# Kernel tuning notes

Measured on AMD Instinct MI355X. Metric: run time of the kernel, lower is better.

## Reference

```python
import jax, jax.numpy as jnp
import numpy as np
from jax import lax

D_MODEL, D_INNER, D_STATE, DT_RANK, KG, DCONV = 96, 96, 64, 6, 4, 3
BATCH, SEQ = 4, 16384


def setup_inputs() -> dict:
    ks = jax.random.split(jax.random.key(0), 8)
    x = jax.random.normal(ks[0], (BATCH, SEQ, D_MODEL), jnp.float32)
    in_proj_w = jax.random.normal(ks[1], (2 * D_INNER, D_MODEL), jnp.float32) * (D_MODEL ** -0.5)
    conv_w = jax.random.normal(ks[2], (D_INNER, 1, DCONV), jnp.float32) * (DCONV ** -0.5)
    x_proj_w = jax.random.normal(ks[3], (KG, DT_RANK + 2 * D_STATE, D_INNER), jnp.float32) * (D_INNER ** -0.5)
    dt_projs_w = 0.1 * jax.random.uniform(ks[4], (KG, D_INNER, DT_RANK), jnp.float32)
    out_proj_w = jax.random.normal(ks[5], (D_MODEL, D_INNER), jnp.float32) * (D_INNER ** -0.5)
    A_logs = 0.1 * jax.random.uniform(ks[6], (KG * D_INNER, D_STATE), jnp.float32)
    Ds = jnp.ones((KG * D_INNER,), jnp.float32)
    return dict(x=x, in_proj_w=in_proj_w, conv_w=conv_w, x_proj_w=x_proj_w,
                dt_projs_w=dt_projs_w, out_proj_w=out_proj_w, A_logs=A_logs, Ds=Ds)


def _forward_core(x, x_proj_w, dt_projs_w, A_logs, Ds):
    # x: (B, L, Din). 4-direction stack: [fwd, rev, fwd, rev] as in torch code.
    B, L, Din = x.shape
    x_rev = jnp.flip(x, axis=1)
    xs = jnp.stack([x, x_rev, x, x_rev], axis=1)                      # (B, K, L, Din)
    x_dbl = jnp.einsum('bkld,kcd->bklc', xs, x_proj_w)                # (B, K, L, R+2N)
    dts, Bs, Cs = jnp.split(x_dbl, [DT_RANK, DT_RANK + D_STATE], axis=-1)
    dts = jnp.einsum('bklr,kdr->bkld', dts, dt_projs_w)               # (B, K, L, Din)
    delta = jax.nn.softplus(dts)                                      # delta_bias is zeros in source
    A = -jnp.exp(A_logs).reshape(KG, D_INNER, D_STATE)                # (K, Din, N)
    D = Ds.reshape(KG, D_INNER)

    def step(h, inp):
        d, u, b, c = inp                                              # d,u:(B,K,Din)  b,c:(B,K,N)
        dA = jnp.exp(d[..., None] * A)                                # (B,K,Din,N)
        h = dA * h + (d * u)[..., None] * b[:, :, None, :]
        y = jnp.einsum('bkdn,bkn->bkd', h, c)
        return h, y

    seq = (jnp.moveaxis(delta, 2, 0), jnp.moveaxis(xs, 2, 0),
           jnp.moveaxis(Bs, 2, 0), jnp.moveaxis(Cs, 2, 0))
    h0 = jnp.zeros((B, KG, D_INNER, D_STATE), x.dtype)
    _, ys = lax.scan(step, h0, seq)                                   # (L, B, K, Din)
    ys = jnp.moveaxis(ys, 0, 2) + D[None, :, None, :] * xs            # (B, K, L, Din)
    # cross-merge: un-flip the reversed directions and sum all 4
    y = ys[:, 0] + jnp.flip(ys[:, 1], axis=1) + ys[:, 2] + jnp.flip(ys[:, 3], axis=1)
    return y                                                          # (B, L, Din)


def reference(x, in_proj_w, conv_w, x_proj_w, dt_projs_w, out_proj_w, A_logs, Ds):
    xz = x @ in_proj_w.T                                              # (B, L, 2*Din)
    xx, z = jnp.split(xz, 2, axis=-1)
    z = jax.nn.gelu(z, approximate=False)
    # depthwise conv1d over the sequence dim, 'same' padding
    pad = (DCONV - 1) // 2
    xc = lax.conv_general_dilated(xx.transpose(0, 2, 1), conv_w, (1,), [(pad, pad)],
                                  dimension_numbers=('NCH', 'OIH', 'NCH'),
                                  feature_group_count=D_INNER)        # (B, Din, L)
    xx = jax.nn.gelu(xc.transpose(0, 2, 1), approximate=False)        # (B, L, Din)
    y = _forward_core(xx, x_proj_w, dt_projs_w, A_logs, Ds)
    y = y * z
    return y @ out_proj_w.T                                           # (B, L, d_model)
```

## Files before the change

kernel.cpp:

```cpp
#include <hip/hip_runtime.h>
#include <hip/hip_bf16.h>
#include <math.h>

#define B_    4
#define L_    16384
#define DM    96
#define DI    96
#define NS    64
#define RK    6
#define KG_   4
#define CDIM  134

#define CL    512
#define NC    32
#define NWARM 64
#define STG   32

typedef float f32x2 __attribute__((ext_vector_type(2)));
typedef float f32x4 __attribute__((ext_vector_type(4)));
typedef short bf16x8 __attribute__((ext_vector_type(8)));

#if defined(__has_builtin)
# if __has_builtin(__builtin_amdgcn_exp2f)
#  define EXP2F(x) __builtin_amdgcn_exp2f(x)
# else
#  define EXP2F(x) exp2f(x)
# endif
#else
# define EXP2F(x) exp2f(x)
#endif

__device__ __forceinline__ float gelu_f(float v) {
  return 0.5f * v * (1.0f + erff(v * 0.70710678118654752f));
}

__device__ __forceinline__ unsigned short f2bf(float v) {
  __hip_bfloat16 h = __float2bfloat16(v);
  return *reinterpret_cast<unsigned short*>(&h);
}

__global__ __launch_bounds__(256) void k_front(
    const float* __restrict__ x, const float* __restrict__ w,
    const float* __restrict__ cw,
    float* __restrict__ xxc, float* __restrict__ zg)
{
  __shared__ __align__(16) char smem[80 * 104 * 2 + 96 * 104 * 2];
  unsigned short* sxb = reinterpret_cast<unsigned short*>(smem);
  unsigned short* swb = reinterpret_cast<unsigned short*>(smem + 80 * 104 * 2);
  const int tid = threadIdx.x;
  const int lt = blockIdx.x, cs = blockIdx.y, b = blockIdx.z;
  const int l0 = lt * 64;
  const int lbase = l0 - 1;

  for (int i = tid; i < 80 * 24; i += 256) {
    const int r = i / 24, q = i % 24;
    int l = lbase + r; l = l < 0 ? 0 : (l >= L_ ? L_ - 1 : l);
    const float4 v = reinterpret_cast<const float4*>(x + ((size_t)b * L_ + l) * DM)[q];
    ushort4 u;
    u.x = f2bf(v.x); u.y = f2bf(v.y); u.z = f2bf(v.z); u.w = f2bf(v.w);
    *reinterpret_cast<ushort4*>(&sxb[r * 104 + q * 4]) = u;
  }
  const float* wp = w + (size_t)cs * 96 * DM;
  for (int i = tid; i < 96 * 24; i += 256) {
    const int r = i / 24, q = i % 24;
    const float4 v = reinterpret_cast<const float4*>(wp + (size_t)r * DM)[q];
    ushort4 u;
    u.x = f2bf(v.x); u.y = f2bf(v.y); u.z = f2bf(v.z); u.w = f2bf(v.w);
    *reinterpret_cast<ushort4*>(&swb[r * 104 + q * 4]) = u;
  }
  __syncthreads();

  const int wv = tid >> 6, lane = tid & 63;
  const int lrow = lane & 15, lkg = lane >> 4;
  f32x4 acc[8];
#pragma unroll
  for (int i = 0; i < 8; ++i) {
    acc[i] = (f32x4){0.f, 0.f, 0.f, 0.f};
    const int tile = wv + 4 * i;
    if (tile < 30) {
      const int mt = tile / 6, nt = tile - mt * 6;
#pragma unroll
      for (int kk = 0; kk < 3; ++kk) {
        const int kbase = kk * 32 + lkg * 8;
        const bf16x8 af = *reinterpret_cast<const bf16x8*>(&sxb[(mt * 16 + lrow) * 104 + kbase]);
        const bf16x8 bfm = *reinterpret_cast<const bf16x8*>(&swb[(nt * 16 + lrow) * 104 + kbase]);
        acc[i] = __builtin_amdgcn_mfma_f32_16x16x32_bf16(af, bfm, acc[i], 0, 0, 0);
      }
    }
  }
  __syncthreads();

  float* sprod = reinterpret_cast<float*>(smem);
#pragma unroll
  for (int i = 0; i < 8; ++i) {
    const int tile = wv + 4 * i;
    if (tile < 30) {
      const int mt = tile / 6, nt = tile - mt * 6;
      const int row = mt * 16 + lkg * 4;
      const int col = nt * 16 + lrow;
#pragma unroll
      for (int reg = 0; reg < 4; ++reg)
        sprod[(row + reg) * 100 + col] = acc[i][reg];
    }
  }
  __syncthreads();

  if (cs == 0) {
    float* op = xxc + ((size_t)b * L_ + l0) * DI;
    for (int i = tid; i < 64 * 24; i += 256) {
      const int ro = i / 24, q = i % 24;
      const int lo = l0 + ro;
      const float4 xm4 = *reinterpret_cast<const float4*>(&sprod[ro * 100 + q * 4]);
      const float4 x04 = *reinterpret_cast<const float4*>(&sprod[(ro + 1) * 100 + q * 4]);
      const float4 xq4 = *reinterpret_cast<const float4*>(&sprod[(ro + 2) * 100 + q * 4]);
      const float mzero = (lo > 0) ? 1.f : 0.f;
      const float qzero = (lo < L_ - 1) ? 1.f : 0.f;
      float4 o;
      {
        const int d0 = q * 4;
        const float* c = cw + d0 * 3;
        o.x = gelu_f(c[0] * xm4.x * mzero + c[1]  * x04.x + c[2]  * xq4.x * qzero);
        o.y = gelu_f(c[3] * xm4.y * mzero + c[4]  * x04.y + c[5]  * xq4.y * qzero);
        o.z = gelu_f(c[6] * xm4.z * mzero + c[7]  * x04.z + c[8]  * xq4.z * qzero);
        o.w = gelu_f(c[9] * xm4.w * mzero + c[10] * x04.w + c[11] * xq4.w * qzero);
      }
      reinterpret_cast<float4*>(op + (size_t)ro * DI)[q] = o;
    }
  } else {
    float* op = zg + ((size_t)b * L_ + l0) * DI;
    for (int i = tid; i < 64 * 24; i += 256) {
      const int ro = i / 24, q = i % 24;
      const float4 v = *reinterpret_cast<const float4*>(&sprod[(ro + 1) * 100 + q * 4]);
      float4 o;
      o.x = gelu_f(v.x); o.y = gelu_f(v.y); o.z = gelu_f(v.z); o.w = gelu_f(v.w);
      reinterpret_cast<float4*>(op + (size_t)ro * DI)[q] = o;
    }
  }
}

__global__ __launch_bounds__(256) void k_xproj(
    const float* __restrict__ xxc, const float* __restrict__ xpw,
    const float* __restrict__ dtw,
    __hip_bfloat16* __restrict__ delta, __hip_bfloat16* __restrict__ Bs,
    __hip_bfloat16* __restrict__ Cs)
{
  __shared__ __align__(16) unsigned short sxb[64][104];
  __shared__ __align__(16) unsigned short swb[144 * 104];
  __shared__ __align__(16) float sdtw[576];
  const int tid = threadIdx.x;
  const int lt = blockIdx.x, kdir = blockIdx.y, b = blockIdx.z;
  const int l0 = lt * 64;
  const bool rev = (kdir & 1) != 0;

  for (int i = tid; i < 576; i += 256) sdtw[i] = dtw[(size_t)kdir * 576 + i];

  for (int i = tid; i < 64 * 24; i += 256) {
    const int r = i / 24, q = i % 24;
    const int l = l0 + r;
    const int p = rev ? (L_ - 1 - l) : l;
    const float4 v = reinterpret_cast<const float4*>(xxc + ((size_t)b * L_ + p) * DI)[q];
    ushort4 u;
    u.x = f2bf(v.x); u.y = f2bf(v.y); u.z = f2bf(v.z); u.w = f2bf(v.w);
    *reinterpret_cast<ushort4*>(&sxb[r][q * 4]) = u;
  }
  const float* wp = xpw + (size_t)kdir * CDIM * DI;
  for (int i = tid; i < 144 * 24; i += 256) {
    const int r = i / 24, q = i % 24;
    float4 v = make_float4(0.f, 0.f, 0.f, 0.f);
    if (r < CDIM) v = reinterpret_cast<const float4*>(wp + (size_t)r * DI)[q];
    ushort4 u;
    u.x = f2bf(v.x); u.y = f2bf(v.y); u.z = f2bf(v.z); u.w = f2bf(v.w);
    *reinterpret_cast<ushort4*>(&swb[r * 104 + q * 4]) = u;
  }
  __syncthreads();

  const int wv = tid >> 6, lane = tid & 63;
  const int m0 = wv * 16;
  const int lrow = lane & 15, lkg = lane >> 4;
  f32x4 acc[9];
#pragma unroll
  for (int n = 0; n < 9; ++n) acc[n] = (f32x4){0.f, 0.f, 0.f, 0.f};

#pragma unroll
  for (int kk = 0; kk < 3; ++kk) {
    const int kbase = kk * 32 + lkg * 8;
    const bf16x8 af = *reinterpret_cast<const bf16x8*>(&sxb[m0 + lrow][kbase]);
#pragma unroll
    for (int n = 0; n < 9; ++n) {
      const bf16x8 bfm = *reinterpret_cast<const bf16x8*>(&swb[(n * 16 + lrow) * 104 + kbase]);
      acc[n] = __builtin_amdgcn_mfma_f32_16x16x32_bf16(af, bfm, acc[n], 0, 0, 0);
    }
  }
  __syncthreads();

  unsigned short* soB = swb;
  unsigned short* soC = swb + 64 * 68;
  float* sdts = reinterpret_cast<float*>(swb + 2 * 64 * 68);

  {
    const int row = m0 + lkg * 4;
#pragma unroll
    for (int n = 0; n < 9; ++n) {
      const int c = n * 16 + lrow;
#pragma unroll
      for (int reg = 0; reg < 4; ++reg) {
        const float v = acc[n][reg];
        const int rr = row + reg;
        if (c < RK)            sdts[rr * 8 + c] = v;
        else if (c < RK + NS)  soB[rr * 68 + (c - RK)] = f2bf(v);
        else if (c < CDIM)     soC[rr * 68 + (c - RK - NS)] = f2bf(v);
      }
    }
  }
  __syncthreads();

  const size_t bk = (size_t)(b * KG_ + kdir);
  {
    unsigned short* bsg = reinterpret_cast<unsigned short*>(Bs);
    unsigned short* csg = reinterpret_cast<unsigned short*>(Cs);
    const size_t nbase = (bk * L_ + l0) * NS;
    for (int i = tid; i < 64 * 16; i += 256) {
      const int r = i >> 4, q = i & 15;
      const ushort4 vb = *reinterpret_cast<const ushort4*>(&soB[r * 68 + q * 4]);
      const ushort4 vc = *reinterpret_cast<const ushort4*>(&soC[r * 68 + q * 4]);
      *reinterpret_cast<ushort4*>(bsg + nbase + (size_t)r * NS + q * 4) = vb;
      *reinterpret_cast<ushort4*>(csg + nbase + (size_t)r * NS + q * 4) = vc;
    }
  }
  {
    unsigned short* dg = reinterpret_cast<unsigned short*>(delta);
    const size_t dbase = (bk * L_ + l0) * DI;
    for (int i = tid; i < 64 * 24; i += 256) {
      const int r = i / 24, q = i - r * 24;
      const int dc0 = q * 4;
      ushort4 u;
      float o[4];
#pragma unroll
      for (int e = 0; e < 4; ++e) {
        const int dc = dc0 + e;
        float s = 0.f;
#pragma unroll
        for (int rr6 = 0; rr6 < RK; ++rr6)
          s += sdts[r * 8 + rr6] * sdtw[dc * RK + rr6];
        o[e] = (s > 20.f) ? s : log1pf(__expf(s));
      }
      u.x = f2bf(o[0]); u.y = f2bf(o[1]); u.z = f2bf(o[2]); u.w = f2bf(o[3]);
      *reinterpret_cast<ushort4*>(dg + dbase + (size_t)r * DI + dc0) = u;
    }
  }
}

__global__ __launch_bounds__(768) void k_scan(
    const float* __restrict__ xxc,
    const __hip_bfloat16* __restrict__ delta,
    const __hip_bfloat16* __restrict__ Bs,
    const __hip_bfloat16* __restrict__ Cs,
    const float* __restrict__ A_logs, const float* __restrict__ Ds,
    float* __restrict__ ysum)
{
  __shared__ __align__(16) float s_du[STG][192];
  __shared__ __align__(16) float s_u[STG][96];
  __shared__ __align__(16) float s_B[STG][64];
  __shared__ __align__(16) float s_C[STG][64];
  __shared__ __align__(16) float s_y[STG][96];
  const int tid = threadIdx.x;
  const int ci = blockIdx.x, k = blockIdx.y, b = blockIdx.z;
  const int d = tid >> 3, j = tid & 7;
  const int jn = j * 8;
  const bool rev = (k & 1) != 0;
  const float LOG2E = 1.4426950408889634f;

  const int r96 = tid / 96;
  const int c96 = tid - r96 * 96;
  const int r64 = tid >> 6;
  const int c64 = tid & 63;

  f32x2 a2[4], h[4];
#pragma unroll
  for (int p = 0; p < 4; ++p) {
    const int n = jn + 2 * p;
    a2[p].x = -__expf(A_logs[((size_t)(k * DI + d)) * NS + n])     * LOG2E;
    a2[p].y = -__expf(A_logs[((size_t)(k * DI + d)) * NS + n + 1]) * LOG2E;
    h[p].x = 0.f; h[p].y = 0.f;
  }
  const float Dc = Ds[k * DI + c96];

  const int emit0 = ci * CL;
  const int lstart = (emit0 - NWARM > 0) ? (emit0 - NWARM) : 0;
  const int lend = emit0 + CL;
  const size_t bk = (size_t)(b * KG_ + k);

  for (int s = lstart; s < lend; s += STG) {
    __syncthreads();
    {
      const size_t dbase = (bk * L_ + s) * DI;
      const int pbase = rev ? (L_ - 1 - s) : s;
      const int psgn  = rev ? -1 : 1;
      const float* ubase = xxc + ((size_t)b * L_ + pbase) * DI + c96;
#pragma unroll
      for (int it = 0; it < 4; ++it) {
        const int t = r96 + 8 * it;
        const float dl = __bfloat162float(delta[dbase + (size_t)t * DI + c96]);
        const float uu = ubase[(ptrdiff_t)psgn * t * DI];
        f32x2 v; v.x = dl; v.y = dl * uu;
        *(f32x2*)&s_du[t][2 * c96] = v;
        s_u[t][c96] = uu;
      }
      const size_t nbase = (bk * L_ + s) * NS;
#pragma unroll
      for (int it = 0; it < 3; ++it) {
        const int t = r64 + 12 * it;
        if (t < STG) {
          s_B[t][c64] = __bfloat162float(Bs[nbase + (size_t)t * NS + c64]);
          s_C[t][c64] = __bfloat162float(Cs[nbase + (size_t)t * NS + c64]);
        }
      }
    }
    __syncthreads();
    const bool emit = (s >= emit0);
#pragma unroll 8
    for (int t = 0; t < STG; ++t) {
      const f32x2 du = *(const f32x2*)&s_du[t][2 * d];
      const float dlt = du.x, bu = du.y;
      const f32x2 dlt2 = {dlt, dlt};
      const f32x2 bu2 = {bu, bu};
      const f32x4 Bv0 = *(const f32x4*)&s_B[t][jn];
      const f32x4 Bv1 = *(const f32x4*)&s_B[t][jn + 4];
      const f32x4 Cv0 = *(const f32x4*)&s_C[t][jn];
      const f32x4 Cv1 = *(const f32x4*)&s_C[t][jn + 4];
      const f32x2 bp[4] = {{Bv0.x, Bv0.y}, {Bv0.z, Bv0.w},
                           {Bv1.x, Bv1.y}, {Bv1.z, Bv1.w}};
      const f32x2 cp[4] = {{Cv0.x, Cv0.y}, {Cv0.z, Cv0.w},
                           {Cv1.x, Cv1.y}, {Cv1.z, Cv1.w}};
      f32x2 y2 = {0.f, 0.f};
#pragma unroll
      for (int p = 0; p < 4; ++p) {
        const f32x2 arg = dlt2 * a2[p];
        f32x2 e;
        e.x = EXP2F(arg.x);
        e.y = EXP2F(arg.y);
        h[p] = e * h[p] + bu2 * bp[p];
        y2 += h[p] * cp[p];
      }
      float y = y2.x + y2.y;
      y += __shfl_xor(y, 1);
      y += __shfl_xor(y, 2);
      y += __shfl_xor(y, 4);
      if (emit && j == 0) s_y[t][d] = y;
    }
    if (emit) {
      __syncthreads();
      const int pbase = rev ? (L_ - 1 - s) : s;
      const int psgn  = rev ? -1 : 1;
      float* ybase = ysum + ((size_t)b * L_ + pbase) * DI + c96;
#pragma unroll
      for (int it = 0; it < 4; ++it) {
        const int t = r96 + 8 * it;
        atomicAdd(ybase + (ptrdiff_t)psgn * t * DI,
                  fmaf(Dc, s_u[t][c96], s_y[t][c96]));
      }
    }
  }
}

__global__ __launch_bounds__(256) void k_out(
    const float* __restrict__ ysum, const float* __restrict__ zg,
    const float* __restrict__ wout, float* __restrict__ out)
{
  __shared__ __align__(16) char smem[64 * 104 * 2 + 96 * 104 * 2];
  unsigned short* sab = reinterpret_cast<unsigned short*>(smem);
  unsigned short* swb = reinterpret_cast<unsigned short*>(smem + 64*104*2);
  const int tid = threadIdx.x;
  const int lt = blockIdx.x, b = blockIdx.y;
  const int l0 = lt * 64;
  const size_t rbase = ((size_t)b * L_ + l0) * DI;

  for (int i = tid; i < 64 * 24; i += 256) {
    const int r = i / 24, q = i % 24;
    float4 av = reinterpret_cast<const float4*>(ysum + rbase + (size_t)r * DI)[q];
    const float4 zv = reinterpret_cast<const float4*>(zg + rbase + (size_t)r * DI)[q];
    ushort4 u;
    u.x = f2bf(av.x * zv.x); u.y = f2bf(av.y * zv.y);
    u.z = f2bf(av.z * zv.z); u.w = f2bf(av.w * zv.w);
    *reinterpret_cast<ushort4*>(&sab[r * 104 + q * 4]) = u;
  }
  for (int i = tid; i < 96 * 24; i += 256) {
    const int r = i / 24, q = i % 24;
    const float4 v = reinterpret_cast<const float4*>(wout + (size_t)r * DM)[q];
    ushort4 u;
    u.x = f2bf(v.x); u.y = f2bf(v.y); u.z = f2bf(v.z); u.w = f2bf(v.w);
    *reinterpret_cast<ushort4*>(&swb[r * 104 + q * 4]) = u;
  }
  __syncthreads();

  const int wv = tid >> 6, lane = tid & 63;
  const int m0 = wv * 16;
  const int lrow = lane & 15, lkg = lane >> 4;
  f32x4 acc[6];
#pragma unroll
  for (int n = 0; n < 6; ++n) acc[n] = (f32x4){0.f, 0.f, 0.f, 0.f};

#pragma unroll
  for (int kk = 0; kk < 3; ++kk) {
    const int kbase = kk * 32 + lkg * 8;
    const bf16x8 af = *reinterpret_cast<const bf16x8*>(&sab[(m0 + lrow) * 104 + kbase]);
#pragma unroll
    for (int n = 0; n < 6; ++n) {
      const bf16x8 bfm = *reinterpret_cast<const bf16x8*>(&swb[(n * 16 + lrow) * 104 + kbase]);
      acc[n] = __builtin_amdgcn_mfma_f32_16x16x32_bf16(af, bfm, acc[n], 0, 0, 0);
    }
  }
  __syncthreads();

  float* sout = reinterpret_cast<float*>(smem);
  {
    const int row = m0 + lkg * 4;
#pragma unroll
    for (int n = 0; n < 6; ++n) {
      const int c = n * 16 + lrow;
#pragma unroll
      for (int reg = 0; reg < 4; ++reg)
        sout[(row + reg) * 100 + c] = acc[n][reg];
    }
  }
  __syncthreads();

  float* op = out + ((size_t)b * L_ + l0) * DM;
  for (int i = tid; i < 64 * 24; i += 256) {
    const int r = i / 24, q = i % 24;
    const float4 v = *reinterpret_cast<const float4*>(&sout[r * 100 + q * 4]);
    reinterpret_cast<float4*>(op + (size_t)r * DM)[q] = v;
  }
}

extern "C" void kernel_launch(void* const* d_in, const int* in_sizes, int n_in,
                              void* d_out, int out_size, void* d_ws, size_t ws_size,
                              hipStream_t stream)
{
  const float* x    = (const float*)d_in[0];
  const float* ipw  = (const float*)d_in[1];
  const float* cw   = (const float*)d_in[2];
  const float* xpw  = (const float*)d_in[3];
  const float* dtw  = (const float*)d_in[4];
  const float* opw  = (const float*)d_in[5];
  const float* alog = (const float*)d_in[6];
  const float* dsv  = (const float*)d_in[7];
  float* out = (float*)d_out;
  char* ws = (char*)d_ws;

  const size_t SZ_XZ  = (size_t)B_ * L_ * 192 * 4;
  const size_t SZ_F   = (size_t)B_ * L_ * DI * 4;
  const size_t SZ_NBF = (size_t)B_ * KG_ * L_ * NS * 2;

  __hip_bfloat16* dlt  = (__hip_bfloat16*)ws;
  float* xxc           = (float*)(ws + SZ_XZ);
  float* zgp           = (float*)(ws + SZ_XZ + SZ_F);
  __hip_bfloat16* Bsp  = (__hip_bfloat16*)(ws + SZ_XZ + 2 * SZ_F);
  __hip_bfloat16* Csp  = (__hip_bfloat16*)(ws + SZ_XZ + 2 * SZ_F + SZ_NBF);
  float* ysum          = (float*)(ws + SZ_XZ + 2 * SZ_F + 2 * SZ_NBF);

  hipMemsetAsync(ysum, 0, SZ_F, stream);
  k_front  <<<dim3(L_ / 64, 2, B_),   256, 0, stream>>>(x, ipw, cw, xxc, zgp);
  k_xproj  <<<dim3(L_ / 64, KG_, B_), 256, 0, stream>>>(xxc, xpw, dtw, dlt, Bsp, Csp);
  k_scan   <<<dim3(NC, KG_, B_),      768, 0, stream>>>(xxc, dlt, Bsp, Csp, alog, dsv, ysum);
  k_out    <<<dim3(L_ / 64, B_),      256, 0, stream>>>(ysum, zgp, opw, out);
}
```

Measured before the change: 480.0 us.

## Fuse in-projection, conv and x-projection into a single front kernel

Merges k_front and k_xproj into one kernel. Each block now computes both the x and z halves of the in-projection, then the conv+GELU, and keeps the conv output in LDS as bf16. It then loops over the four scan directions, handling reversed directions by remapping rows instead of re-reading flipped xxc from global memory. This removes a kernel launch, the global re-read of xxc (four times), and the duplicate x-tile loading across the two channel halves. In exchange the grid shrinks to a quarter, LDS use per block rises to about 57 KB, and the direction loop serialises the x_proj weight loads with extra barriers, which lowers occupancy and parallelism.

```diff
diff --git a/kernel.cpp b/kernel.cpp
--- a/kernel.cpp
+++ b/kernel.cpp
@@ -39,18 +39,24 @@
   return *reinterpret_cast<unsigned short*>(&h);
 }
 
-__global__ __launch_bounds__(256) void k_front(
+__global__ __launch_bounds__(256) void k_fx(
     const float* __restrict__ x, const float* __restrict__ w,
-    const float* __restrict__ cw,
-    float* __restrict__ xxc, float* __restrict__ zg)
+    const float* __restrict__ cw, const float* __restrict__ xpw,
+    const float* __restrict__ dtw,
+    float* __restrict__ xxc, float* __restrict__ zg,
+    __hip_bfloat16* __restrict__ delta, __hip_bfloat16* __restrict__ Bs,
+    __hip_bfloat16* __restrict__ Cs)
 {
-  __shared__ __align__(16) char smem[80 * 104 * 2 + 96 * 104 * 2];
-  unsigned short* sxb = reinterpret_cast<unsigned short*>(smem);
-  unsigned short* swb = reinterpret_cast<unsigned short*>(smem + 80 * 104 * 2);
+  __shared__ __align__(16) char smem[57600];
+  unsigned short* sxb  = reinterpret_cast<unsigned short*>(smem);
+  unsigned short* swbX = reinterpret_cast<unsigned short*>(smem + 16640);
+  unsigned short* swbZ = reinterpret_cast<unsigned short*>(smem + 36608);
   const int tid = threadIdx.x;
-  const int lt = blockIdx.x, cs = blockIdx.y, b = blockIdx.z;
+  const int lt = blockIdx.x, b = blockIdx.y;
   const int l0 = lt * 64;
   const int lbase = l0 - 1;
+  const int wv = tid >> 6, lane = tid & 63;
+  const int lrow = lane & 15, lkg = lane >> 4;
 
   for (int i = tid; i < 80 * 24; i += 256) {
     const int r = i / 24, q = i % 24;
@@ -60,22 +66,23 @@
     u.x = f2bf(v.x); u.y = f2bf(v.y); u.z = f2bf(v.z); u.w = f2bf(v.w);
     *reinterpret_cast<ushort4*>(&sxb[r * 104 + q * 4]) = u;
   }
-  const float* wp = w + (size_t)cs * 96 * DM;
   for (int i = tid; i < 96 * 24; i += 256) {
     const int r = i / 24, q = i % 24;
-    const float4 v = reinterpret_cast<const float4*>(wp + (size_t)r * DM)[q];
-    ushort4 u;
-    u.x = f2bf(v.x); u.y = f2bf(v.y); u.z = f2bf(v.z); u.w = f2bf(v.w);
-    *reinterpret_cast<ushort4*>(&swb[r * 104 + q * 4]) = u;
-  }
-  __syncthreads();
-
-  const int wv = tid >> 6, lane = tid & 63;
-  const int lrow = lane & 15, lkg = lane >> 4;
-  f32x4 acc[8];
+    const float4 vx = reinterpret_cast<const float4*>(w + (size_t)r * DM)[q];
+    const float4 vz = reinterpret_cast<const float4*>(w + (size_t)(96 + r) * DM)[q];
+    ushort4 ux, uz;
+    ux.x = f2bf(vx.x); ux.y = f2bf(vx.y); ux.z = f2bf(vx.z); ux.w = f2bf(vx.w);
+    uz.x = f2bf(vz.x); uz.y = f2bf(vz.y); uz.z = f2bf(vz.z); uz.w = f2bf(vz.w);
+    *reinterpret_cast<ushort4*>(&swbX[r * 104 + q * 4]) = ux;
+    *reinterpret_cast<ushort4*>(&swbZ[r * 104 + q * 4]) = uz;
+  }
+  __syncthreads();
+
+  f32x4 accX[8], accZ[8];
 #pragma unroll
   for (int i = 0; i < 8; ++i) {
-    acc[i] = (f32x4){0.f, 0.f, 0.f, 0.f};
+    accX[i] = (f32x4){0.f, 0.f, 0.f, 0.f};
+    accZ[i] = (f32x4){0.f, 0.f, 0.f, 0.f};
     const int tile = wv + 4 * i;
     if (tile < 30) {
       const int mt = tile / 6, nt = tile - mt * 6;
@@ -83,14 +90,17 @@
       for (int kk = 0; kk < 3; ++kk) {
         const int kbase = kk * 32 + lkg * 8;
         const bf16x8 af = *reinterpret_cast<const bf16x8*>(&sxb[(mt * 16 + lrow) * 104 + kbase]);
-        const bf16x8 bfm = *reinterpret_cast<const bf16x8*>(&swb[(nt * 16 + lrow) * 104 + kbase]);
-        acc[i] = __builtin_amdgcn_mfma_f32_16x16x32_bf16(af, bfm, acc[i], 0, 0, 0);
-      }
-    }
-  }
-  __syncthreads();
-
-  float* sprod = reinterpret_cast<float*>(smem);
+        const bf16x8 bx = *reinterpret_cast<const bf16x8*>(&swbX[(nt * 16 + lrow) * 104 + kbase]);
+        const bf16x8 bz = *reinterpret_cast<const bf16x8*>(&swbZ[(nt * 16 + lrow) * 104 + kbase]);
+        accX[i] = __builtin_amdgcn_mfma_f32_16x16x32_bf16(af, bx, accX[i], 0, 0, 0);
+        accZ[i] = __builtin_amdgcn_mfma_f32_16x16x32_bf16(af, bz, accZ[i], 0, 0, 0);
+      }
+    }
+  }
+  __syncthreads();
+
+  float* prodX = reinterpret_cast<float*>(smem);
+  float* prodZ = reinterpret_cast<float*>(smem + 32000);
 #pragma unroll
   for (int i = 0; i < 8; ++i) {
     const int tile = wv + 4 * i;
@@ -99,20 +109,36 @@
       const int row = mt * 16 + lkg * 4;
       const int col = nt * 16 + lrow;
 #pragma unroll
-      for (int reg = 0; reg < 4; ++reg)
-        sprod[(row + reg) * 100 + col] = acc[i][reg];
-    }
-  }
-  __syncthreads();
-
-  if (cs == 0) {
+      for (int reg = 0; reg < 4; ++reg) {
+        prodX[(row + reg) * 100 + col] = accX[i][reg];
+        const int zr = row + reg - 1;
+        if (zr >= 0 && zr < 64) prodZ[zr * 100 + col] = accZ[i][reg];
+      }
+    }
+  }
+  __syncthreads();
+
+  {
+    float* op = zg + ((size_t)b * L_ + l0) * DI;
+    for (int i = tid; i < 64 * 24; i += 256) {
+      const int ro = i / 24, q = i % 24;
+      const float4 v = *reinterpret_cast<const float4*>(&prodZ[ro * 100 + q * 4]);
+      float4 o;
+      o.x = gelu_f(v.x); o.y = gelu_f(v.y); o.z = gelu_f(v.z); o.w = gelu_f(v.w);
+      reinterpret_cast<float4*>(op + (size_t)ro * DI)[q] = o;
+    }
+  }
+  __syncthreads();
+
+  unsigned short* sxc = reinterpret_cast<unsigned short*>(smem + 32000);
+  {
     float* op = xxc + ((size_t)b * L_ + l0) * DI;
     for (int i = tid; i < 64 * 24; i += 256) {
       const int ro = i / 24, q = i % 24;
       const int lo = l0 + ro;
-      const float4 xm4 = *reinterpret_cast<const float4*>(&sprod[ro * 100 + q * 4]);
-      const float4 x04 = *reinterpret_cast<const float4*>(&sprod[(ro + 1) * 100 + q * 4]);
-      const float4 xq4 = *reinterpret_cast<const float4*>(&sprod[(ro + 2) * 100 + q * 4]);
+      const float4 xm4 = *reinterpret_cast<const float4*>(&prodX[ro * 100 + q * 4]);
+      const float4 x04 = *reinterpret_cast<const float4*>(&prodX[(ro + 1) * 100 + q * 4]);
+      const float4 xq4 = *reinterpret_cast<const float4*>(&prodX[(ro + 2) * 100 + q * 4]);
       const float mzero = (lo > 0) ? 1.f : 0.f;
       const float qzero = (lo < L_ - 1) ? 1.f : 0.f;
       float4 o;
@@ -125,127 +151,103 @@
         o.w = gelu_f(c[9] * xm4.w * mzero + c[10] * x04.w + c[11] * xq4.w * qzero);
       }
       reinterpret_cast<float4*>(op + (size_t)ro * DI)[q] = o;
-    }
-  } else {
-    float* op = zg + ((size_t)b * L_ + l0) * DI;
-    for (int i = tid; i < 64 * 24; i += 256) {
-      const int ro = i / 24, q = i % 24;
-      const float4 v = *reinterpret_cast<const float4*>(&sprod[(ro + 1) * 100 + q * 4]);
-      float4 o;
-      o.x = gelu_f(v.x); o.y = gelu_f(v.y); o.z = gelu_f(v.z); o.w = gelu_f(v.w);
-      reinterpret_cast<float4*>(op + (size_t)ro * DI)[q] = o;
-    }
-  }
-}
-
-__global__ __launch_bounds__(256) void k_xproj(
-    const float* __restrict__ xxc, const float* __restrict__ xpw,
-    const float* __restrict__ dtw,
-    __hip_bfloat16* __restrict__ delta, __hip_bfloat16* __restrict__ Bs,
-    __hip_bfloat16* __restrict__ Cs)
-{
-  __shared__ __align__(16) unsigned short sxb[64][104];
-  __shared__ __align__(16) unsigned short swb[144 * 104];
-  __shared__ __align__(16) float sdtw[576];
-  const int tid = threadIdx.x;
-  const int lt = blockIdx.x, kdir = blockIdx.y, b = blockIdx.z;
-  const int l0 = lt * 64;
-  const bool rev = (kdir & 1) != 0;
-
-  for (int i = tid; i < 576; i += 256) sdtw[i] = dtw[(size_t)kdir * 576 + i];
-
-  for (int i = tid; i < 64 * 24; i += 256) {
-    const int r = i / 24, q = i % 24;
-    const int l = l0 + r;
-    const int p = rev ? (L_ - 1 - l) : l;
-    const float4 v = reinterpret_cast<const float4*>(xxc + ((size_t)b * L_ + p) * DI)[q];
-    ushort4 u;
-    u.x = f2bf(v.x); u.y = f2bf(v.y); u.z = f2bf(v.z); u.w = f2bf(v.w);
-    *reinterpret_cast<ushort4*>(&sxb[r][q * 4]) = u;
-  }
-  const float* wp = xpw + (size_t)kdir * CDIM * DI;
-  for (int i = tid; i < 144 * 24; i += 256) {
-    const int r = i / 24, q = i % 24;
-    float4 v = make_float4(0.f, 0.f, 0.f, 0.f);
-    if (r < CDIM) v = reinterpret_cast<const float4*>(wp + (size_t)r * DI)[q];
-    ushort4 u;
-    u.x = f2bf(v.x); u.y = f2bf(v.y); u.z = f2bf(v.z); u.w = f2bf(v.w);
-    *reinterpret_cast<ushort4*>(&swb[r * 104 + q * 4]) = u;
-  }
-  __syncthreads();
-
-  const int wv = tid >> 6, lane = tid & 63;
+      ushort4 u;
+      u.x = f2bf(o.x); u.y = f2bf(o.y); u.z = f2bf(o.z); u.w = f2bf(o.w);
+      *reinterpret_cast<ushort4*>(&sxc[ro * 104 + q * 4]) = u;
+    }
+  }
+
+  unsigned short* sWk  = reinterpret_cast<unsigned short*>(smem);
+  float*          sdtw = reinterpret_cast<float*>(smem + 45312);
   const int m0 = wv * 16;
-  const int lrow = lane & 15, lkg = lane >> 4;
-  f32x4 acc[9];
-#pragma unroll
-  for (int n = 0; n < 9; ++n) acc[n] = (f32x4){0.f, 0.f, 0.f, 0.f};
-
-#pragma unroll
-  for (int kk = 0; kk < 3; ++kk) {
-    const int kbase = kk * 32 + lkg * 8;
-    const bf16x8 af = *reinterpret_cast<const bf16x8*>(&sxb[m0 + lrow][kbase]);
-#pragma unroll
-    for (int n = 0; n < 9; ++n) {
-      const bf16x8 bfm = *reinterpret_cast<const bf16x8*>(&swb[(n * 16 + lrow) * 104 + kbase]);
-      acc[n] = __builtin_amdgcn_mfma_f32_16x16x32_bf16(af, bfm, acc[n], 0, 0, 0);
-    }
-  }
-  __syncthreads();
-
-  unsigned short* soB = swb;
-  unsigned short* soC = swb + 64 * 68;
-  float* sdts = reinterpret_cast<float*>(swb + 2 * 64 * 68);
-
-  {
-    const int row = m0 + lkg * 4;
-#pragma unroll
-    for (int n = 0; n < 9; ++n) {
-      const int c = n * 16 + lrow;
-#pragma unroll
-      for (int reg = 0; reg < 4; ++reg) {
-        const float v = acc[n][reg];
-        const int rr = row + reg;
-        if (c < RK)            sdts[rr * 8 + c] = v;
-        else if (c < RK + NS)  soB[rr * 68 + (c - RK)] = f2bf(v);
-        else if (c < CDIM)     soC[rr * 68 + (c - RK - NS)] = f2bf(v);
-      }
-    }
-  }
-  __syncthreads();
-
-  const size_t bk = (size_t)(b * KG_ + kdir);
-  {
-    unsigned short* bsg = reinterpret_cast<unsigned short*>(Bs);
-    unsigned short* csg = reinterpret_cast<unsigned short*>(Cs);
-    const size_t nbase = (bk * L_ + l0) * NS;
-    for (int i = tid; i < 64 * 16; i += 256) {
-      const int r = i >> 4, q = i & 15;
-      const ushort4 vb = *reinterpret_cast<const ushort4*>(&soB[r * 68 + q * 4]);
-      const ushort4 vc = *reinterpret_cast<const ushort4*>(&soC[r * 68 + q * 4]);
-      *reinterpret_cast<ushort4*>(bsg + nbase + (size_t)r * NS + q * 4) = vb;
-      *reinterpret_cast<ushort4*>(csg + nbase + (size_t)r * NS + q * 4) = vc;
-    }
-  }
-  {
-    unsigned short* dg = reinterpret_cast<unsigned short*>(delta);
-    const size_t dbase = (bk * L_ + l0) * DI;
-    for (int i = tid; i < 64 * 24; i += 256) {
-      const int r = i / 24, q = i - r * 24;
-      const int dc0 = q * 4;
-      ushort4 u;
-      float o[4];
-#pragma unroll
-      for (int e = 0; e < 4; ++e) {
-        const int dc = dc0 + e;
-        float s = 0.f;
-#pragma unroll
-        for (int rr6 = 0; rr6 < RK; ++rr6)
-          s += sdts[r * 8 + rr6] * sdtw[dc * RK + rr6];
-        o[e] = (s > 20.f) ? s : log1pf(__expf(s));
-      }
-      u.x = f2bf(o[0]); u.y = f2bf(o[1]); u.z = f2bf(o[2]); u.w = f2bf(o[3]);
-      *reinterpret_cast<ushort4*>(dg + dbase + (size_t)r * DI + dc0) = u;
+  for (int kdir = 0; kdir < 4; ++kdir) {
+    const bool rev = (kdir & 1) != 0;
+    __syncthreads();
+    {
+      const float* wp = xpw + (size_t)kdir * CDIM * DI;
+      for (int i = tid; i < 144 * 24; i += 256) {
+        const int r = i / 24, q = i % 24;
+        float4 v = make_float4(0.f, 0.f, 0.f, 0.f);
+        if (r < CDIM) v = reinterpret_cast<const float4*>(wp + (size_t)r * DI)[q];
+        ushort4 u;
+        u.x = f2bf(v.x); u.y = f2bf(v.y); u.z = f2bf(v.z); u.w = f2bf(v.w);
+        *reinterpret_cast<ushort4*>(&sWk[r * 104 + q * 4]) = u;
+      }
+      for (int i = tid; i < 576; i += 256) sdtw[i] = dtw[(size_t)kdir * 576 + i];
+    }
+    __syncthreads();
+
+    f32x4 acc[9];
+#pragma unroll
+    for (int n = 0; n < 9; ++n) acc[n] = (f32x4){0.f, 0.f, 0.f, 0.f};
+#pragma unroll
+    for (int kk = 0; kk < 3; ++kk) {
+      const int kbase = kk * 32 + lkg * 8;
+      const bf16x8 af = *reinterpret_cast<const bf16x8*>(&sxc[(m0 + lrow) * 104 + kbase]);
+#pragma unroll
+      for (int n = 0; n < 9; ++n) {
+        const bf16x8 bfm = *reinterpret_cast<const bf16x8*>(&sWk[(n * 16 + lrow) * 104 + kbase]);
+        acc[n] = __builtin_amdgcn_mfma_f32_16x16x32_bf16(af, bfm, acc[n], 0, 0, 0);
+      }
+    }
+    __syncthreads();
+
+    unsigned short* soB = reinterpret_cast<unsigned short*>(smem);
+    unsigned short* soC = reinterpret_cast<unsigned short*>(smem + 8704);
+    float*          sdts = reinterpret_cast<float*>(smem + 17408);
+    {
+      const int row = m0 + lkg * 4;
+#pragma unroll
+      for (int n = 0; n < 9; ++n) {
+        const int c = n * 16 + lrow;
+#pragma unroll
+        for (int reg = 0; reg < 4; ++reg) {
+          const float v = acc[n][reg];
+          const int rr = row + reg;
+          if (c < RK)            sdts[rr * 8 + c] = v;
+          else if (c < RK + NS)  soB[rr * 68 + (c - RK)] = f2bf(v);
+          else if (c < CDIM)     soC[rr * 68 + (c - RK - NS)] = f2bf(v);
+        }
+      }
+    }
+    __syncthreads();
+
+    const size_t bk = (size_t)(b * KG_ + kdir);
+    const int base_l = rev ? (L_ - 64 - l0) : l0;
+    {
+      unsigned short* bsg = reinterpret_cast<unsigned short*>(Bs);
+      unsigned short* csg = reinterpret_cast<unsigned short*>(Cs);
+      const size_t nbase = (bk * L_ + base_l) * NS;
+      for (int i = tid; i < 64 * 16; i += 256) {
+        const int r = i >> 4, q = i & 15;
+        const int ri = rev ? (63 - r) : r;
+        const ushort4 vb = *reinterpret_cast<const ushort4*>(&soB[ri * 68 + q * 4]);
+        const ushort4 vc = *reinterpret_cast<const ushort4*>(&soC[ri * 68 + q * 4]);
+        *reinterpret_cast<ushort4*>(bsg + nbase + (size_t)r * NS + q * 4) = vb;
+        *reinterpret_cast<ushort4*>(csg + nbase + (size_t)r * NS + q * 4) = vc;
+      }
+    }
+    {
+      unsigned short* dg = reinterpret_cast<unsigned short*>(delta);
+      const size_t dbase = (bk * L_ + base_l) * DI;
+      for (int i = tid; i < 64 * 24; i += 256) {
+        const int r = i / 24, q = i - r * 24;
+        const int ri = rev ? (63 - r) : r;
+        const int dc0 = q * 4;
+        ushort4 u;
+        float o[4];
+#pragma unroll
+        for (int e = 0; e < 4; ++e) {
+          const int dc = dc0 + e;
+          float s = 0.f;
+#pragma unroll
+          for (int rr6 = 0; rr6 < RK; ++rr6)
+            s += sdts[ri * 8 + rr6] * sdtw[dc * RK + rr6];
+          o[e] = (s > 20.f) ? s : log1pf(__expf(s));
+        }
+        u.x = f2bf(o[0]); u.y = f2bf(o[1]); u.z = f2bf(o[2]); u.w = f2bf(o[3]);
+        *reinterpret_cast<ushort4*>(dg + dbase + (size_t)r * DI + dc0) = u;
+      }
     }
   }
 }
@@ -460,8 +462,8 @@
   float* ysum          = (float*)(ws + SZ_XZ + 2 * SZ_F + 2 * SZ_NBF);
 
   hipMemsetAsync(ysum, 0, SZ_F, stream);
-  k_front  <<<dim3(L_ / 64, 2, B_),   256, 0, stream>>>(x, ipw, cw, xxc, zgp);
-  k_xproj  <<<dim3(L_ / 64, KG_, B_), 256, 0, stream>>>(xxc, xpw, dtw, dlt, Bsp, Csp);
-  k_scan   <<<dim3(NC, KG_, B_),      768, 0, stream>>>(xxc, dlt, Bsp, Csp, alog, dsv, ysum);
-  k_out    <<<dim3(L_ / 64, B_),      256, 0, stream>>>(ysum, zgp, opw, out);
-}
+  k_fx     <<<dim3(L_ / 64, B_),  256, 0, stream>>>(x, ipw, cw, xpw, dtw,
+                                                    xxc, zgp, dlt, Bsp, Csp);
+  k_scan   <<<dim3(NC, KG_, B_),  768, 0, stream>>>(xxc, dlt, Bsp, Csp, alog, dsv, ysum);
+  k_out    <<<dim3(L_ / 64, B_),  256, 0, stream>>>(ysum, zgp, opw, out);
+}
```

After: 498.1 us. +3.8%, slower.
